# Kernel tuning notes

Measured on AMD Instinct MI355X. Metric: run time of the kernel, lower is better.

The kernel has to match this reference:

```python
import jax, jax.numpy as jnp
import numpy as np

NUM_HEADS = 16

def setup_inputs() -> dict:
    key = jax.random.key(0)
    ks = jax.random.split(key, 7)
    b, sq, sk, d = 2, 2048, 2048, 1024
    return {
        "query": jax.random.normal(ks[0], (b, sq, d), dtype=jnp.float32),
        "key": jax.random.normal(ks[1], (b, sk, d), dtype=jnp.float32),
        "value": jax.random.normal(ks[2], (b, sk, d), dtype=jnp.float32),
        "key_mask": jax.random.randint(ks[3], (b, sk, 1), 0, 2, dtype=jnp.int32),
        "query_mask": jax.random.randint(ks[4], (b, sq, 1), 0, 2, dtype=jnp.int32),
        "Wo": jax.random.normal(ks[5], (d, d), dtype=jnp.float32) * 0.02,
        "bo": jnp.zeros((d,), dtype=jnp.float32),
    }

def reference(query, key, value, key_mask, query_mask, Wo, bo):
    b, s_q, d = query.shape
    s_k = key.shape[1]
    h = NUM_HEADS
    hd = d // h
    q = query.reshape(b, s_q, h, hd).transpose(0, 2, 1, 3)   # [b,h,sq,hd]
    k = key.reshape(b, s_k, h, hd).transpose(0, 2, 1, 3)     # [b,h,sk,hd]
    v = value.reshape(b, s_k, h, hd).transpose(0, 2, 1, 3)   # [b,h,sk,hd]
    scores = jnp.einsum('bhqd,bhkd->bhqk', q, k) / jnp.sqrt(jnp.float32(hd))
    # dual masking: key_mask [b,sk,1] -> [b,1,1,sk]; query_mask [b,sq,1] -> [b,1,sq,1]
    km = (key_mask[:, :, 0] != 0)[:, None, None, :]
    qm = (query_mask[:, :, 0] != 0)[:, None, :, None]
    valid = km & qm                                           # [b,1,sq,sk]
    scores = jnp.where(valid, scores, -jnp.inf)
    # safe softmax: fully-masked rows -> softmax over zeros, then zeroed out
    # (matches torch: softmax over all -inf gives NaN, nan_to_num -> 0.0)
    row_valid = jnp.any(valid, axis=-1, keepdims=True)        # [b,1,sq,1]
    safe_scores = jnp.where(row_valid, scores, 0.0)
    w = jax.nn.softmax(safe_scores, axis=-1)
    w = jnp.where(row_valid, w, 0.0)
    # dropout is identity (eval mode / p=0)
    out = jnp.einsum('bhqk,bhkd->bhqd', w, v)                 # [b,h,sq,hd]
    out = out.transpose(0, 2, 1, 3).reshape(b, s_q, d)
    return out @ Wo.T + bo
```

## Files before the change

kernel.cpp:

```cpp
#include <hip/hip_runtime.h>

typedef __bf16 bfv8 __attribute__((ext_vector_type(8)));
typedef float f32x4 __attribute__((ext_vector_type(4)));
typedef short s16x8 __attribute__((ext_vector_type(8)));
typedef unsigned int u32;
typedef unsigned int u32x4 __attribute__((ext_vector_type(4)));

#define MFMA16(a,b,c) __builtin_amdgcn_mfma_f32_16x16x32_bf16((a),(b),(c),0,0,0)

__device__ __forceinline__ u32 pk2(float a, float b){
  u32 r; asm("v_cvt_pk_bf16_f32 %0, %1, %2" : "=v"(r) : "v"(a), "v"(b)); return r;
}
__device__ __forceinline__ bfv8 cvt8s(const float* p, float s){
  u32x4 r;
  #pragma unroll
  for (int j=0;j<4;++j) r[j] = pk2(p[2*j]*s, p[2*j+1]*s);
  return *(bfv8*)&r;
}
__device__ __forceinline__ void glds16(const short* g, short* l){
  __builtin_amdgcn_global_load_lds(
      (const __attribute__((address_space(1))) u32*)g,
      (__attribute__((address_space(3))) u32*)l, 16, 0, 0);
}

__global__ __launch_bounds__(256) void prep(const float* __restrict__ K, const float* __restrict__ V,
                                            const float* __restrict__ Wo, const int* __restrict__ km,
                                            short* __restrict__ Kt, short* __restrict__ Vt,
                                            short* __restrict__ Wb, short* __restrict__ kms){
  __shared__ short tl[64][65];
  const int bid = blockIdx.x, tid = threadIdx.x;
  if (bid < 2048){
    int idx = bid*256 + tid;
    int cs = idx & 7, r = (idx >> 3) & 63, kt = (idx >> 9) & 31, bh = idx >> 14;
    int b = bh >> 4, h = bh & 15;
    int c = cs ^ (r & 7);
    const float* src = K + ((size_t)(b*2048 + kt*64 + r))*1024 + h*64 + c*8;
    float4 a = ((const float4*)src)[0], bb = ((const float4*)src)[1];
    u32x4 o;
    o[0]=pk2(a.x,a.y); o[1]=pk2(a.z,a.w); o[2]=pk2(bb.x,bb.y); o[3]=pk2(bb.z,bb.w);
    ((u32x4*)Kt)[idx] = o;
  } else if (bid < 3072){
    int vb = bid - 2048;
    int kt = vb & 31, bh = vb >> 5;
    int b = bh >> 4, h = bh & 15;
    {
      int s = tid >> 2, d0 = (tid & 3) * 16;
      float kmv = (km[b*2048 + kt*64 + s] != 0) ? 1.0f : 0.0f;
      const float* src = V + ((size_t)(b*2048 + kt*64 + s))*1024 + h*64 + d0;
      #pragma unroll
      for (int j = 0; j < 4; ++j){
        float4 v = ((const float4*)src)[j];
        tl[d0+4*j+0][s] = (short)(pk2(v.x*kmv, 0.f) & 0xffff);
        tl[d0+4*j+1][s] = (short)(pk2(v.y*kmv, 0.f) & 0xffff);
        tl[d0+4*j+2][s] = (short)(pk2(v.z*kmv, 0.f) & 0xffff);
        tl[d0+4*j+3][s] = (short)(pk2(v.w*kmv, 0.f) & 0xffff);
      }
    }
    __syncthreads();
    {
      int r = tid >> 2, cp = (tid & 3) * 2;
      short* dst = Vt + (((size_t)(bh*32 + kt)*64 + r) << 6);
      #pragma unroll
      for (int q = 0; q < 2; ++q){
        int cs = cp + q;
        int c = cs ^ (r & 7);
        s16x8 o;
        #pragma unroll
        for (int j = 0; j < 8; ++j){
          int s = c*8 + j;
          int sg = s >> 2, rr = s & 3;
          int t = (sg >> 3)*2 + (sg & 1);
          int a = (sg >> 1) & 3;
          int kap = t*16 + a*4 + rr;
          o[j] = tl[r][kap];
        }
        *(s16x8*)(dst + cs*8) = o;
      }
    }
  } else if (bid < 3584){
    int i = (bid - 3072)*256 + tid;
    const float* p = Wo + (size_t)i*8;
    u32x4 o;
    o[0]=pk2(p[0],p[1]); o[1]=pk2(p[2],p[3]); o[2]=pk2(p[4],p[5]); o[3]=pk2(p[6],p[7]);
    ((u32x4*)Wb)[i] = o;
  } else {
    int i = (bid - 3584)*256 + tid;
    if (i < 4096){
      int bb = i >> 11, kt = (i >> 6) & 31, s = i & 63;
      int rr = s & 3, a = (s >> 3) & 3, t = ((s >> 5) & 1)*2 + ((s >> 2) & 1);
      int key = t*16 + a*4 + rr;
      kms[i] = (km[bb*2048 + kt*64 + key] != 0) ? (short)0x3F80 : (short)0;
    }
  }
}

__global__ __launch_bounds__(512, 4) void attn8(const short* __restrict__ Kt, const short* __restrict__ Vt,
                                                const float* __restrict__ Qf, const short* __restrict__ kms,
                                                const int* __restrict__ qmask, short* __restrict__ X){
  __shared__ __align__(16) short kl[4][64][64];
  __shared__ __align__(16) short vl[4][64][64];
  __shared__ __align__(16) short kml[32][64];
  const int wid = blockIdx.x;
  const int bh = (wid & 7)*4 + (wid >> 7);
  const int qt = (wid >> 3) & 15;
  const int b = bh >> 4, h = bh & 15;
  const int tid = threadIdx.x;
  const int w = tid >> 6, lane = tid & 63, lo = lane & 15, hi = lane >> 4;
  const int toff = (wid * 7) & 31;

  const f32x4 ZERO4 = {0.f, 0.f, 0.f, 0.f};
  const float QSCALE = 0.125f * 1.44269504088896f;
  const int qrow = qt*128 + w*16 + lo;
  bfv8 qf0, qf1;
  {
    const float* qp = Qf + ((size_t)(b*2048 + qrow))*1024 + h*64 + hi*8;
    qf0 = cvt8s(qp, QSCALE);
    qf1 = cvt8s(qp + 32, QSCALE);
  }

  if (w < 4) glds16(kms + b*2048 + w*512 + lane*8, &kml[0][0] + w*512);
  asm volatile("s_waitcnt vmcnt(0)" ::: "memory");
  __builtin_amdgcn_s_barrier();
  __builtin_amdgcn_sched_barrier(0);

  const short* ktb = Kt + ((size_t)(bh*32) << 12);
  const short* vtb = Vt + ((size_t)(bh*32) << 12);
  const int sgoff = w*512 + lane*8;
  const int csK   = (hi ^ (lo & 7)) * 8;

  f32x4 acc[4];
  #pragma unroll
  for (int t2=0;t2<4;++t2) acc[t2] = ZERO4;
  f32x4 accL = ZERO4;

  #pragma unroll
  for (int p = 0; p < 3; ++p){
    const int tp = (toff + p) & 31;
    glds16(ktb + ((size_t)tp << 12) + sgoff, &kl[p][0][0] + w*512);
    asm volatile("" ::: "memory");
    glds16(vtb + ((size_t)tp << 12) + sgoff, &vl[p][0][0] + w*512);
    asm volatile("" ::: "memory");
  }

  for (int i = 0; i < 32; ++i){
    asm volatile("s_waitcnt vmcnt(4)" ::: "memory");
    __builtin_amdgcn_s_barrier();
    __builtin_amdgcn_sched_barrier(0);
    {
      const int tn = (toff + i + 3) & 31, bn = (i + 3) & 3;
      glds16(ktb + ((size_t)tn << 12) + sgoff, &kl[bn][0][0] + w*512);
      asm volatile("" ::: "memory");
      glds16(vtb + ((size_t)tn << 12) + sgoff, &vl[bn][0][0] + w*512);
      asm volatile("" ::: "memory");
    }
    const short (*kc)[64] = kl[i & 3];
    const short (*vc)[64] = vl[i & 3];
    const int tcur = (toff + i) & 31;
    const short* kmrow = &kml[tcur][0];
    bfv8 kmf0 = *(const bfv8*)(kmrow + hi*8);
    bfv8 kmf1 = *(const bfv8*)(kmrow + 32 + hi*8);

    u32 pk[8];
    __builtin_amdgcn_s_setprio(1);
    #pragma unroll
    for (int t=0;t<4;++t){
      const short* rowp = &kc[t*16+lo][0];
      bfv8 kf0 = *(const bfv8*)(rowp + csK);
      bfv8 kf1 = *(const bfv8*)(rowp + (csK ^ 32));
      f32x4 c = MFMA16(kf0, qf0, ZERO4);
      c = MFMA16(kf1, qf1, c);
      float p0 = __builtin_amdgcn_exp2f(c[0]);
      float p1 = __builtin_amdgcn_exp2f(c[1]);
      float p2 = __builtin_amdgcn_exp2f(c[2]);
      float p3 = __builtin_amdgcn_exp2f(c[3]);
      pk[2*t]   = pk2(p0, p1);
      pk[2*t+1] = pk2(p2, p3);
    }
    __builtin_amdgcn_s_setprio(0);
    u32x4 pw0 = {pk[0],pk[1],pk[2],pk[3]};
    u32x4 pw1 = {pk[4],pk[5],pk[6],pk[7]};
    bfv8 pb0 = *(bfv8*)&pw0, pb1 = *(bfv8*)&pw1;

    __builtin_amdgcn_s_setprio(1);
    accL = MFMA16(kmf0, pb0, accL);
    accL = MFMA16(kmf1, pb1, accL);
    #pragma unroll
    for (int t2=0;t2<4;++t2){
      const short* rowp = &vc[t2*16+lo][0];
      bfv8 vf0 = *(const bfv8*)(rowp + csK);
      bfv8 vf1 = *(const bfv8*)(rowp + (csK ^ 32));
      acc[t2] = MFMA16(vf0, pb0, acc[t2]);
      acc[t2] = MFMA16(vf1, pb1, acc[t2]);
    }
    __builtin_amdgcn_s_setprio(0);
  }
  asm volatile("s_waitcnt vmcnt(0)" ::: "memory");

  float l = accL[0];
  float inv = (l > 0.f) ? 1.0f/l : 0.f;
  if (qmask[b*2048 + qrow] == 0) inv = 0.f;
  u32* xp = (u32*)(X + ((size_t)(b*2048 + qrow))*1024 + h*64);
  #pragma unroll
  for (int t2=0;t2<4;++t2){
    xp[t2*8 + 2*hi]     = pk2(acc[t2][0]*inv, acc[t2][1]*inv);
    xp[t2*8 + 2*hi + 1] = pk2(acc[t2][2]*inv, acc[t2][3]*inv);
  }
}

__global__ __launch_bounds__(512, 1) void proj4(const short* __restrict__ X, const short* __restrict__ Wb,
                                                const float* __restrict__ bo, float* __restrict__ Y){
  __shared__ __align__(16) short xl[4][128][32];
  __shared__ __align__(16) short wl[4][128][32];
  const int bid = blockIdx.x;
  const int xcd = bid & 7, ii = bid >> 3;
  const int by = xcd*4 + (ii >> 3);
  const int bx = ii & 7;
  const int tid = threadIdx.x;
  const int w = tid >> 6, lane = tid & 63, lo = lane & 15, hi = lane >> 4;
  const int wr = w >> 2, wc = w & 3;
  const int brow = by*128, bcol = bx*128;
  const f32x4 ZERO4 = {0.f, 0.f, 0.f, 0.f};

  const int ci = w*64 + lane;
  const int rX = ci >> 2, csX = ci & 3;
  const short* xs = X  + (size_t)(brow + rX)*1024 + ((csX ^ (rX & 3)))*8;
  const short* ws = Wb + (size_t)(bcol + rX)*1024 + ((csX ^ (rX & 3)))*8;
  const int csA = (hi ^ (lo & 3)) * 8;

  f32x4 acc[4][2];
  #pragma unroll
  for (int i=0;i<4;++i){ acc[i][0] = ZERO4; acc[i][1] = ZERO4; }

  #pragma unroll
  for (int p = 0; p < 3; ++p){
    glds16(xs + p*32, &xl[p][0][0] + w*512);
    asm volatile("" ::: "memory");
    glds16(ws + p*32, &wl[p][0][0] + w*512);
    asm volatile("" ::: "memory");
  }

  for (int kt = 0; kt < 32; ++kt){
    asm volatile("s_waitcnt vmcnt(4)" ::: "memory");
    __builtin_amdgcn_s_barrier();
    __builtin_amdgcn_sched_barrier(0);
    {
      const int tn = (kt + 3) & 31, bn = (kt + 3) & 3;
      glds16(xs + tn*32, &xl[bn][0][0] + w*512);
      asm volatile("" ::: "memory");
      glds16(ws + tn*32, &wl[bn][0][0] + w*512);
      asm volatile("" ::: "memory");
    }
    const short* xc  = &xl[kt & 3][0][0];
    const short* wcp = &wl[kt & 3][0][0];
    bfv8 a[4], bb[2];
    #pragma unroll
    for (int i=0;i<4;++i) a[i]  = *(const bfv8*)(xc  + (wr*64 + i*16 + lo)*32 + csA);
    #pragma unroll
    for (int j=0;j<2;++j) bb[j] = *(const bfv8*)(wcp + (wc*32 + j*16 + lo)*32 + csA);
    __builtin_amdgcn_s_setprio(1);
    #pragma unroll
    for (int i=0;i<4;++i){
      acc[i][0] = MFMA16(a[i], bb[0], acc[i][0]);
      acc[i][1] = MFMA16(a[i], bb[1], acc[i][1]);
    }
    __builtin_amdgcn_s_setprio(0);
  }
  asm volatile("s_waitcnt vmcnt(0)" ::: "memory");

  float bv[2];
  bv[0] = bo[bcol + wc*32 + lo];
  bv[1] = bo[bcol + wc*32 + 16 + lo];
  #pragma unroll
  for (int i=0;i<4;++i){
    #pragma unroll
    for (int r=0;r<4;++r){
      size_t row = (size_t)(brow + wr*64 + i*16 + hi*4 + r);
      float* yp = Y + row*1024 + bcol + wc*32 + lo;
      yp[0]  = acc[i][0][r] + bv[0];
      yp[16] = acc[i][1][r] + bv[1];
    }
  }
}

extern "C" void kernel_launch(void* const* d_in, const int* in_sizes, int n_in,
                              void* d_out, int out_size, void* d_ws, size_t ws_size,
                              hipStream_t stream){
  const float* Q   = (const float*)d_in[0];
  const float* K   = (const float*)d_in[1];
  const float* V   = (const float*)d_in[2];
  const int* key_mask   = (const int*)d_in[3];
  const int* query_mask = (const int*)d_in[4];
  const float* Wo  = (const float*)d_in[5];
  const float* bo  = (const float*)d_in[6];

  short* Ktw = (short*)d_ws;
  short* Vtw = Ktw + 4194304;
  short* Wb  = Vtw + 4194304;
  short* Xb  = Wb + 1048576;
  short* kms = Xb + 4194304;

  prep<<<3600,256,0,stream>>>(K, V, Wo, key_mask, Ktw, Vtw, Wb, kms);
  attn8<<<512,512,0,stream>>>(Ktw, Vtw, Q, kms, query_mask, Xb);
  proj4<<<256,512,0,stream>>>(Xb, Wb, bo, (float*)d_out);
}
```

Measured before the change: 77.37 us.

## Read K/V tiles directly from global memory instead of LDS pipeline

Removes the LDS multi-buffered global_load_lds pipeline and its per-iteration barriers in the attention kernel, with each wave loading K and V fragments straight from global memory. The swizzle is dropped from the prep layout because loads no longer go through LDS. Blocks shrink to 4 waves covering 64 query rows, so 1024 blocks are launched. The kernel now depends on L1/L2 caching to share K/V tiles across waves, and global load latency is exposed inside the loop because nothing prefetches ahead.

```diff
diff --git a/kernel.cpp b/kernel.cpp
--- a/kernel.cpp
+++ b/kernel.cpp
@@ -33,8 +33,7 @@
     int idx = bid*256 + tid;
     int cs = idx & 7, r = (idx >> 3) & 63, kt = (idx >> 9) & 31, bh = idx >> 14;
     int b = bh >> 4, h = bh & 15;
-    int c = cs ^ (r & 7);
-    const float* src = K + ((size_t)(b*2048 + kt*64 + r))*1024 + h*64 + c*8;
+    const float* src = K + ((size_t)(b*2048 + kt*64 + r))*1024 + h*64 + cs*8;
     float4 a = ((const float4*)src)[0], bb = ((const float4*)src)[1];
     u32x4 o;
     o[0]=pk2(a.x,a.y); o[1]=pk2(a.z,a.w); o[2]=pk2(bb.x,bb.y); o[3]=pk2(bb.z,bb.w);
@@ -63,11 +62,10 @@
       #pragma unroll
       for (int q = 0; q < 2; ++q){
         int cs = cp + q;
-        int c = cs ^ (r & 7);
         s16x8 o;
         #pragma unroll
         for (int j = 0; j < 8; ++j){
-          int s = c*8 + j;
+          int s = cs*8 + j;
           int sg = s >> 2, rr = s & 3;
           int t = (sg >> 3)*2 + (sg & 1);
           int a = (sg >> 1) & 3;
@@ -94,15 +92,12 @@
   }
 }
 
-__global__ __launch_bounds__(512, 4) void attn8(const short* __restrict__ Kt, const short* __restrict__ Vt,
-                                                const float* __restrict__ Qf, const short* __restrict__ kms,
-                                                const int* __restrict__ qmask, short* __restrict__ X){
-  __shared__ __align__(16) short kl[4][64][64];
-  __shared__ __align__(16) short vl[4][64][64];
-  __shared__ __align__(16) short kml[32][64];
+__global__ __launch_bounds__(256) void attn15(const short* __restrict__ Kt, const short* __restrict__ Vt,
+                                              const float* __restrict__ Qf, const short* __restrict__ kms,
+                                              const int* __restrict__ qmask, short* __restrict__ X){
   const int wid = blockIdx.x;
-  const int bh = (wid & 7)*4 + (wid >> 7);
-  const int qt = (wid >> 3) & 15;
+  const int bh = (wid & 7)*4 + (wid >> 8);
+  const int qt = (wid >> 3) & 31;
   const int b = bh >> 4, h = bh & 15;
   const int tid = threadIdx.x;
   const int w = tid >> 6, lane = tid & 63, lo = lane & 15, hi = lane >> 4;
@@ -110,7 +105,7 @@
 
   const f32x4 ZERO4 = {0.f, 0.f, 0.f, 0.f};
   const float QSCALE = 0.125f * 1.44269504088896f;
-  const int qrow = qt*128 + w*16 + lo;
+  const int qrow = qt*64 + w*16 + lo;
   bfv8 qf0, qf1;
   {
     const float* qp = Qf + ((size_t)(b*2048 + qrow))*1024 + h*64 + hi*8;
@@ -118,45 +113,21 @@
     qf1 = cvt8s(qp + 32, QSCALE);
   }
 
-  if (w < 4) glds16(kms + b*2048 + w*512 + lane*8, &kml[0][0] + w*512);
-  asm volatile("s_waitcnt vmcnt(0)" ::: "memory");
-  __builtin_amdgcn_s_barrier();
-  __builtin_amdgcn_sched_barrier(0);
-
   const short* ktb = Kt + ((size_t)(bh*32) << 12);
   const short* vtb = Vt + ((size_t)(bh*32) << 12);
-  const int sgoff = w*512 + lane*8;
-  const int csK   = (hi ^ (lo & 7)) * 8;
+  const short* kmb = kms + b*2048;
+  const int ro  = lo*64 + hi*8;
 
   f32x4 acc[4];
   #pragma unroll
   for (int t2=0;t2<4;++t2) acc[t2] = ZERO4;
   f32x4 accL = ZERO4;
 
-  #pragma unroll
-  for (int p = 0; p < 3; ++p){
-    const int tp = (toff + p) & 31;
-    glds16(ktb + ((size_t)tp << 12) + sgoff, &kl[p][0][0] + w*512);
-    asm volatile("" ::: "memory");
-    glds16(vtb + ((size_t)tp << 12) + sgoff, &vl[p][0][0] + w*512);
-    asm volatile("" ::: "memory");
-  }
-
   for (int i = 0; i < 32; ++i){
-    asm volatile("s_waitcnt vmcnt(4)" ::: "memory");
-    __builtin_amdgcn_s_barrier();
-    __builtin_amdgcn_sched_barrier(0);
-    {
-      const int tn = (toff + i + 3) & 31, bn = (i + 3) & 3;
-      glds16(ktb + ((size_t)tn << 12) + sgoff, &kl[bn][0][0] + w*512);
-      asm volatile("" ::: "memory");
-      glds16(vtb + ((size_t)tn << 12) + sgoff, &vl[bn][0][0] + w*512);
-      asm volatile("" ::: "memory");
-    }
-    const short (*kc)[64] = kl[i & 3];
-    const short (*vc)[64] = vl[i & 3];
     const int tcur = (toff + i) & 31;
-    const short* kmrow = &kml[tcur][0];
+    const short* kT = ktb + ((size_t)tcur << 12);
+    const short* vT = vtb + ((size_t)tcur << 12);
+    const short* kmrow = kmb + tcur*64;
     bfv8 kmf0 = *(const bfv8*)(kmrow + hi*8);
     bfv8 kmf1 = *(const bfv8*)(kmrow + 32 + hi*8);
 
@@ -164,9 +135,9 @@
     __builtin_amdgcn_s_setprio(1);
     #pragma unroll
     for (int t=0;t<4;++t){
-      const short* rowp = &kc[t*16+lo][0];
-      bfv8 kf0 = *(const bfv8*)(rowp + csK);
-      bfv8 kf1 = *(const bfv8*)(rowp + (csK ^ 32));
+      const short* krow = kT + t*1024 + ro;
+      bfv8 kf0 = *(const bfv8*)(krow);
+      bfv8 kf1 = *(const bfv8*)(krow + 32);
       f32x4 c = MFMA16(kf0, qf0, ZERO4);
       c = MFMA16(kf1, qf1, c);
       float p0 = __builtin_amdgcn_exp2f(c[0]);
@@ -186,15 +157,14 @@
     accL = MFMA16(kmf1, pb1, accL);
     #pragma unroll
     for (int t2=0;t2<4;++t2){
-      const short* rowp = &vc[t2*16+lo][0];
-      bfv8 vf0 = *(const bfv8*)(rowp + csK);
-      bfv8 vf1 = *(const bfv8*)(rowp + (csK ^ 32));
+      const short* vrow = vT + t2*1024 + ro;
+      bfv8 vf0 = *(const bfv8*)(vrow);
+      bfv8 vf1 = *(const bfv8*)(vrow + 32);
       acc[t2] = MFMA16(vf0, pb0, acc[t2]);
       acc[t2] = MFMA16(vf1, pb1, acc[t2]);
     }
     __builtin_amdgcn_s_setprio(0);
   }
-  asm volatile("s_waitcnt vmcnt(0)" ::: "memory");
 
   float l = accL[0];
   float inv = (l > 0.f) ? 1.0f/l : 0.f;
@@ -300,6 +270,6 @@
   short* kms = Xb + 4194304;
 
   prep<<<3600,256,0,stream>>>(K, V, Wo, key_mask, Ktw, Vtw, Wb, kms);
-  attn8<<<512,512,0,stream>>>(Ktw, Vtw, Q, kms, query_mask, Xb);
+  attn15<<<1024,256,0,stream>>>(Ktw, Vtw, Q, kms, query_mask, Xb);
   proj4<<<256,512,0,stream>>>(Xb, Wb, bo, (float*)d_out);
 }
```

Measured after the change: 269.2 us. +248.0%, slower.
